# Kernel tuning notes

Hardware: AMD Instinct MI355X
Metric: run time of the kernel (lower is better)

Reference implementation:

```python
import jax, jax.numpy as jnp
import numpy as np

B, S, V, E, H, K = 64, 512, 50000, 128, 256, 20
PAD_IDX, SOS_IDX = 0, 19
NEG = -9999.0


def _lstm_dir(x, mask, W_ih, W_hh, b):
    # x: [B,S,E], mask: [B,S] float. PyTorch gate order: i,f,g,o.
    xg = jnp.einsum('bse,ge->bsg', x, W_ih) + b  # [B,S,4H]

    def step(carry, inp):
        h, c = carry
        xg_t, m = inp  # [B,4H], [B,1]
        g = xg_t + h @ W_hh.T
        i, f, gg, o = jnp.split(g, 4, axis=-1)
        i = jax.nn.sigmoid(i); f = jax.nn.sigmoid(f); o = jax.nn.sigmoid(o)
        gg = jnp.tanh(gg)
        c_new = f * c + i * gg
        h_new = o * jnp.tanh(c_new)
        h = m * h_new + (1.0 - m) * h
        c = m * c_new + (1.0 - m) * c
        return (h, c), h * m  # packed/pad_packed => zeros at padding

    h0 = jnp.zeros((x.shape[0], W_hh.shape[1]), x.dtype)
    _, hs = jax.lax.scan(step, (h0, h0), (xg.transpose(1, 0, 2), mask.T[:, :, None]))
    return hs.transpose(1, 0, 2)  # [B,S,H]


def setup_inputs() -> dict:
    key = jax.random.key(0)
    ks = jax.random.split(key, 12)
    word_seq = jax.random.randint(ks[0], (B, S), 0, V)
    tags = jax.random.randint(ks[1], (B, S), 1, K - 1)  # avoid pad(0) and sos(K-1)
    lengths = S // 2 + jax.random.randint(ks[2], (B,), 0, S // 2)
    sc = 0.1
    embed = jax.random.normal(ks[3], (V, E), jnp.float32) * sc
    W_ih_f = jax.random.normal(ks[4], (4 * H, E), jnp.float32) * sc
    W_hh_f = jax.random.normal(ks[5], (4 * H, H), jnp.float32) * sc
    b_f = jnp.zeros((4 * H,), jnp.float32).at[H:2 * H].set(1.0)  # forget bias 1
    W_ih_b = jax.random.normal(ks[6], (4 * H, E), jnp.float32) * sc
    W_hh_b = jax.random.normal(ks[7], (4 * H, H), jnp.float32) * sc
    b_b = jnp.zeros((4 * H,), jnp.float32).at[H:2 * H].set(1.0)
    lin_W = jax.random.normal(ks[8], (K, 2 * H), jnp.float32) * sc
    lin_b = jnp.zeros((K,), jnp.float32)
    trans = jax.random.normal(ks[9], (K, K), jnp.float32) * 0.1 - 1.0
    trans = trans.at[SOS_IDX, :].set(NEG).at[:, PAD_IDX].set(NEG)
    trans = trans.at[PAD_IDX, :].set(NEG).at[PAD_IDX, PAD_IDX].set(0.0)
    return dict(word_seq=word_seq, tags=tags, lengths=lengths, embed=embed,
                W_ih_f=W_ih_f, W_hh_f=W_hh_f, b_f=b_f,
                W_ih_b=W_ih_b, W_hh_b=W_hh_b, b_b=b_b,
                lin_W=lin_W, lin_b=lin_b, trans=trans)


def reference(word_seq, tags, lengths, embed, W_ih_f, W_hh_f, b_f,
              W_ih_b, W_hh_b, b_b, lin_W, lin_b, trans):
    mask = (jnp.arange(S)[None, :] < lengths[:, None]).astype(jnp.float32)  # [B,S]
    x = embed[word_seq]  # [B,S,E]

    # forward direction
    h_f = _lstm_dir(x, mask, W_ih_f, W_hh_f, b_f)
    # backward direction: reverse within each valid length (packed-seq semantics)
    t = jnp.arange(S)[None, :]
    ri = jnp.where(t < lengths[:, None], lengths[:, None] - 1 - t, t)  # [B,S]
    x_rev = jnp.take_along_axis(x, ri[:, :, None], axis=1)
    h_b_rev = _lstm_dir(x_rev, mask, W_ih_b, W_hh_b, b_b)
    h_b = jnp.take_along_axis(h_b_rev, ri[:, :, None], axis=1)

    rnn_out = jnp.concatenate([h_f, h_b], axis=-1)  # [B,S,2H]
    feats = jnp.einsum('bsd,kd->bsk', rnn_out, lin_W) + lin_b  # [B,S,K]

    # --- CRF numerator: score of gold path ---
    states = jnp.concatenate(
        [jnp.full((B, 1), SOS_IDX, dtype=tags.dtype), tags], axis=1)  # [B,S+1]
    emis = jnp.take_along_axis(feats, tags[:, :, None], axis=-1)[..., 0]  # [B,S]
    trn = trans[states[:, 1:], states[:, :-1]]  # [B,S]
    numerator = jnp.sum((emis + trn) * mask, axis=1)  # [B]

    # --- CRF denominator: forward algorithm (log partition) ---
    score0 = jnp.full((B, K), NEG, jnp.float32).at[:, SOS_IDX].set(0.0)

    def step(score, inp):
        em, m = inp  # [B,K], [B,1]
        new = jax.nn.logsumexp(
            score[:, None, :] + em[:, :, None] + trans[None, :, :], axis=-1)
        score = m * new + (1.0 - m) * score
        return score, None

    score, _ = jax.lax.scan(
        step, score0, (feats.transpose(1, 0, 2), mask.T[:, :, None]))
    denominator = jax.nn.logsumexp(score, axis=-1)  # [B]

    return denominator - numerator  # per-example negative log-likelihood [B]
```

## Files before the change

### kernel.cpp

```cpp
#include <hip/hip_runtime.h>
#include <hip/hip_fp16.h>
#include <stdint.h>

#define BB 64
#define SS 512
#define EE 128
#define HH 256
#define KK 20
#define NEGV -9999.0f
#define SOS_IDX 19

#define VC 18
#define LC 9
#define SC 5

typedef unsigned int u32;

__device__ __forceinline__ float sigm(float x){ return 1.0f / (1.0f + __expf(-x)); }
__device__ __forceinline__ float tanh_fast(float x){
  float e = __expf(2.f * x);
  return 1.f - 2.f / (e + 1.f);
}

__device__ __forceinline__ void pk4(uint4 w, const __half2* hp,
                                    __half2& a0, __half2& a1, __half2& a2, __half2& a3){
  __half2 w0 = *(__half2*)&w.x, w1 = *(__half2*)&w.y, w2 = *(__half2*)&w.z, w3 = *(__half2*)&w.w;
  a0 = __hfma2(w0, hp[0], a0);
  a1 = __hfma2(w1, hp[1], a1);
  a2 = __hfma2(w2, hp[2], a2);
  a3 = __hfma2(w3, hp[3], a3);
}
__device__ __forceinline__ float flushacc(__half2& a0, __half2& a1, __half2& a2, __half2& a3){
  float2 f0 = __half22float2(a0), f1 = __half22float2(a1);
  float2 f2 = __half22float2(a2), f3 = __half22float2(a3);
  __half2 z = __floats2half2_rn(0.f, 0.f);
  a0 = z; a1 = z; a2 = z; a3 = z;
  return ((f0.x + f0.y) + (f1.x + f1.y)) + ((f2.x + f2.y) + (f3.x + f3.y));
}

__global__ void prep_whh(const float* __restrict__ whh_f, const float* __restrict__ whh_b,
                         __half* __restrict__ wp){
  int id = blockIdx.x * 256 + threadIdx.x;
  if (id >= 524288) return;
  int d = id >> 18;
  int rem = id & 262143;
  int row = rem >> 8;
  int k = rem & 255;
  const float* w = d ? whh_b : whh_f;
  wp[(((size_t)d * 32 + (k >> 3)) * 1024 + row) * 8 + (k & 7)] = __float2half(w[row * 256 + k]);
}

__global__ void prep_wih(const float* __restrict__ wih_f, const float* __restrict__ wih_b,
                         float* __restrict__ wt){
  int id = blockIdx.x * 256 + threadIdx.x;
  if (id >= 262144) return;
  int d = id >> 17;
  int rem = id & 131071;
  int col = rem >> 7;
  int k = rem & 127;
  const float* w = d ? wih_b : wih_f;
  wt[(size_t)k * 2048 + d * 1024 + col] = w[col * 128 + k];
}

__global__ __launch_bounds__(256) void xg_gemm(const int* __restrict__ word_seq,
    const int* __restrict__ lengths,
    const float* __restrict__ embed, const float* __restrict__ wt,
    const float* __restrict__ b_f, const float* __restrict__ b_b,
    __half* __restrict__ xg){
  __shared__ __align__(16) float xs[16][128];
  int rb = blockIdx.x >> 1, cb = blockIdx.x & 1;
  {
    int s0 = (rb * 16) & 511, bq = (rb * 16) >> 9;
    if (s0 >= lengths[bq]) return;
  }
  int tid = threadIdx.x;
  {
    int r = tid >> 4, kq = (tid & 15) * 8;
    int bs = rb * 16 + r;
    int w = word_seq[bs];
    const float* er = embed + (size_t)w * 128 + kq;
    float4 a = *(const float4*)er;
    float4 b = *(const float4*)(er + 4);
    *(float4*)&xs[r][kq] = a;
    *(float4*)&xs[r][kq + 4] = b;
  }
  __syncthreads();
  int co = tid * 4;
  const float* bias = cb ? b_b : b_f;
  float4 bv = *(const float4*)(bias + co);
  float4 acc[16];
  #pragma unroll
  for (int r = 0; r < 16; r++) acc[r] = bv;
  const float* wptr = wt + cb * 1024 + co;
  for (int k = 0; k < 128; k++){
    float4 w4 = *(const float4*)(wptr + (size_t)k * 2048);
    #pragma unroll
    for (int r = 0; r < 16; r++){
      float xv = xs[r][k];
      acc[r].x += xv * w4.x; acc[r].y += xv * w4.y;
      acc[r].z += xv * w4.z; acc[r].w += xv * w4.w;
    }
  }
  __half* base = xg + (size_t)cb * ((size_t)BB * SS * 1024);
  #pragma unroll
  for (int r = 0; r < 16; r++){
    int bs = rb * 16 + r;
    __half* o = base + (size_t)bs * 1024 + co;
    __half2 p0 = __floats2half2_rn(acc[r].x, acc[r].y);
    __half2 p1 = __floats2half2_rn(acc[r].z, acc[r].w);
    uint2 st; st.x = *(u32*)&p0; st.y = *(u32*)&p1;
    *(uint2*)o = st;
  }
}

__global__ __launch_bounds__(1024, 4) void lstm_seq(const int* __restrict__ lengths,
    const __half* __restrict__ wp, const __half* __restrict__ xg,
    __half* __restrict__ rnn){
  extern __shared__ __align__(16) char smem[];
  u32*    wl = (u32*)smem;
  float*  gl = (float*)(smem + 147456);
  __half* hb = (__half*)(smem + 151552);

  int bx = blockIdx.x;
  int b = bx & 63, d = bx >> 6;
  int tid = threadIdx.x;
  int u = tid & 255, g = tid >> 8;
  int l = lengths[b];
  const uint4* wp4 = (const uint4*)(wp + (size_t)d * (32 * 1024 * 8));

  uint4 w[VC];
  #pragma unroll
  for (int c = 0; c < VC; c++) w[c] = wp4[c * 1024 + tid];
  #pragma unroll
  for (int c = 0; c < LC; c++)
    *(uint4*)&wl[(c * 1024 + tid) * 4] = wp4[(VC + c) * 1024 + tid];
  if (tid < 256) hb[tid] = __float2half(0.f);
  float cc = 0.f;
  const __half* xgd = xg + ((size_t)d * BB * SS + (size_t)b * SS) * 1024;
  __half* rbp = rnn + (size_t)b * SS * 512 + d * 256;
  int cur = 0;
  __syncthreads();

  for (int t = 0; t < l; t++){
    int s = d ? (l - 1 - t) : t;
    float xv = __half2float(xgd[(size_t)s * 1024 + tid]);
    uint4 sw[SC];
    #pragma unroll
    for (int c = 0; c < SC; c++) sw[c] = wp4[(VC + LC + c) * 1024 + tid];

    const __half* hc = &hb[cur * 256];
    __half2 z = __floats2half2_rn(0.f, 0.f);
    __half2 a0 = z, a1 = z, a2 = z, a3 = z;
    float fa;
    #pragma unroll
    for (int c = 0; c < 16; c++){
      uint4 hv = *(const uint4*)&hc[c * 8];
      pk4(w[c], (const __half2*)&hv, a0, a1, a2, a3);
    }
    fa = flushacc(a0, a1, a2, a3);
    #pragma unroll
    for (int c = 16; c < VC; c++){
      uint4 hv = *(const uint4*)&hc[c * 8];
      pk4(w[c], (const __half2*)&hv, a0, a1, a2, a3);
    }
    #pragma unroll
    for (int c = 0; c < LC; c++){
      uint4 hv = *(const uint4*)&hc[(VC + c) * 8];
      uint4 wv = *(const uint4*)&wl[(c * 1024 + tid) * 4];
      pk4(wv, (const __half2*)&hv, a0, a1, a2, a3);
    }
    #pragma unroll
    for (int c = 0; c < SC; c++){
      uint4 hv = *(const uint4*)&hc[(VC + LC + c) * 8];
      pk4(sw[c], (const __half2*)&hv, a0, a1, a2, a3);
    }
    fa += flushacc(a0, a1, a2, a3);
    fa += xv;

    float gv = (g == 2) ? tanh_fast(fa) : sigm(fa);
    gl[tid] = gv;
    __syncthreads();
    float iv = gl[u], fv = gl[u + 256], ggv = gl[u + 512], ov = gl[u + 768];
    cc = fv * cc + iv * ggv;
    float h = ov * tanh_fast(cc);
    if (g == 0)      hb[(cur ^ 1) * 256 + u] = __float2half(h);
    else if (g == 1) rbp[(size_t)s * 512 + u] = __float2half(h);
    __syncthreads();
    cur ^= 1;
  }
}

__global__ void feat_gemv(const int* __restrict__ lengths,
    const __half* __restrict__ rnn,
    const float* __restrict__ linW, const float* __restrict__ linb,
    float* __restrict__ feats){
  int id = blockIdx.x * 256 + threadIdx.x;
  if (id >= BB * SS * KK) return;
  int row = id / 20;
  int col = id - row * 20;
  int s = row & 511, bq = row >> 9;
  if (s >= lengths[bq]) return;
  const __half* rr = rnn + (size_t)row * 512;
  const float* wr = linW + col * 512;
  float acc = linb[col];
  for (int k8 = 0; k8 < 64; k8++){
    uint4 rv = *(const uint4*)(rr + k8 * 8);
    const __half2* h2 = (const __half2*)&rv;
    float2 p0 = __half22float2(h2[0]);
    float2 p1 = __half22float2(h2[1]);
    float2 p2 = __half22float2(h2[2]);
    float2 p3 = __half22float2(h2[3]);
    float4 wa = *(const float4*)(wr + k8 * 8);
    float4 wb = *(const float4*)(wr + k8 * 8 + 4);
    acc += p0.x * wa.x + p0.y * wa.y + p1.x * wa.z + p1.y * wa.w
         + p2.x * wb.x + p2.y * wb.y + p3.x * wb.z + p3.y * wb.w;
  }
  feats[id] = acc;
}

__global__ __launch_bounds__(64) void crf_kernel(const int* __restrict__ tags,
    const int* __restrict__ lengths, const float* __restrict__ trans,
    const float* __restrict__ feats, float* __restrict__ out){
  int b = blockIdx.x, tid = threadIdx.x;
  __shared__ float tr[400];
  __shared__ float sc[20];
  for (int i = tid; i < 400; i += 64) tr[i] = trans[i];
  __syncthreads();
  int l = lengths[b];
  const int* tg = tags + b * SS;
  const float* fb = feats + (size_t)b * SS * 20;
  float p = 0.f;
  for (int s = tid; s < SS; s += 64){
    if (s < l){
      int cur = tg[s];
      int prev = s ? tg[s - 1] : SOS_IDX;
      p += fb[s * 20 + cur] + tr[cur * 20 + prev];
    }
  }
  #pragma unroll
  for (int off = 32; off; off >>= 1) p += __shfl_down(p, off);
  if (tid < 20) sc[tid] = (tid == SOS_IDX) ? 0.f : NEGV;
  float em = (tid < 20 && l > 0) ? fb[tid] : 0.f;
  for (int s = 0; s < l; s++){
    float em_nxt = (tid < 20 && (s + 1) < l) ? fb[(s + 1) * 20 + tid] : 0.f;
    if (tid < 20){
      const float* trow = &tr[tid * 20];
      float v[20];
      float m = -1e30f;
      #pragma unroll
      for (int jj = 0; jj < 20; jj++){ v[jj] = sc[jj] + trow[jj]; m = fmaxf(m, v[jj]); }
      float ssum = 0.f;
      #pragma unroll
      for (int jj = 0; jj < 20; jj++) ssum += __expf(v[jj] - m);
      sc[tid] = em + m + __logf(ssum);
    }
    em = em_nxt;
  }
  if (tid == 0){
    float m = -1e30f;
    #pragma unroll
    for (int i = 0; i < 20; i++) m = fmaxf(m, sc[i]);
    float ssum = 0.f;
    #pragma unroll
    for (int i = 0; i < 20; i++) ssum += __expf(sc[i] - m);
    out[b] = (m + __logf(ssum)) - p;
  }
}

extern "C" void kernel_launch(void* const* d_in, const int* in_sizes, int n_in,
                              void* d_out, int out_size, void* d_ws, size_t ws_size,
                              hipStream_t stream){
  const int*   word_seq = (const int*)d_in[0];
  const int*   tags     = (const int*)d_in[1];
  const int*   lengths  = (const int*)d_in[2];
  const float* embed    = (const float*)d_in[3];
  const float* wih_f    = (const float*)d_in[4];
  const float* whh_f    = (const float*)d_in[5];
  const float* b_f      = (const float*)d_in[6];
  const float* wih_b    = (const float*)d_in[7];
  const float* whh_b    = (const float*)d_in[8];
  const float* b_b      = (const float*)d_in[9];
  const float* linW     = (const float*)d_in[10];
  const float* linb     = (const float*)d_in[11];
  const float* trans    = (const float*)d_in[12];
  float* out = (float*)d_out;

  char* ws = (char*)d_ws;
  __half* wp    = (__half*)ws;
  float*  wt    = (float*)(ws + (1ull << 20));
  __half* xg    = (__half*)(ws + (2ull << 20));
  __half* rnn   = (__half*)(ws + (2ull << 20) + (128ull << 20));
  float*  feats = (float*)(ws + (2ull << 20) + (160ull << 20));

  (void)hipFuncSetAttribute((const void*)lstm_seq,
        hipFuncAttributeMaxDynamicSharedMemorySize, 152576);

  prep_whh<<<dim3(2048), dim3(256), 0, stream>>>(whh_f, whh_b, wp);
  prep_wih<<<dim3(1024), dim3(256), 0, stream>>>(wih_f, wih_b, wt);
  xg_gemm<<<dim3(4096), dim3(256), 0, stream>>>(word_seq, lengths, embed, wt, b_f, b_b, xg);
  lstm_seq<<<dim3(128), dim3(1024), 152576, stream>>>(lengths, wp, xg, rnn);
  feat_gemv<<<dim3(2560), dim3(256), 0, stream>>>(lengths, rnn, linW, linb, feats);
  crf_kernel<<<dim3(64), dim3(64), 0, stream>>>(tags, lengths, trans, feats, out);
}
```

Measured before the change: 1.690 ms.

## Compute two gate rows per thread in LSTM recurrence, exchange gates via shuffle

The recurrent LSTM kernel moves from 1024 threads (one gate row each) to 512 threads that each compute two gate rows, paired so the i/f/g/o gates for one hidden unit sit in adjacent lanes and are exchanged with __shfl_xor. This drops the shared-memory gate buffer and one __syncthreads per timestep, and tanh is expressed through a scaled sigmoid to avoid divergence. The register/LDS/streamed split of W_hh is rebalanced (more in registers, fewer in LDS) and asm pins keep the weights resident. The cost is higher register pressure per thread and half as many threads to hide latency.

```diff
diff --git a/kernel.cpp b/kernel.cpp
--- a/kernel.cpp
+++ b/kernel.cpp
@@ -10,11 +10,13 @@
 #define NEGV -9999.0f
 #define SOS_IDX 19
 
-#define VC 18
-#define LC 9
+#define VC 20
+#define LC 7
 #define SC 5
 
 typedef unsigned int u32;
+
+#define PIN4(v) asm volatile("" : "+v"((v).x), "+v"((v).y), "+v"((v).z), "+v"((v).w))
 
 __device__ __forceinline__ float sigm(float x){ return 1.0f / (1.0f + __expf(-x)); }
 __device__ __forceinline__ float tanh_fast(float x){
@@ -113,78 +115,100 @@
   }
 }
 
-__global__ __launch_bounds__(1024, 4) void lstm_seq(const int* __restrict__ lengths,
+__global__ __launch_bounds__(512, 2) void lstm_seq(const int* __restrict__ lengths,
     const __half* __restrict__ wp, const __half* __restrict__ xg,
     __half* __restrict__ rnn){
   extern __shared__ __align__(16) char smem[];
   u32*    wl = (u32*)smem;
-  float*  gl = (float*)(smem + 147456);
-  __half* hb = (__half*)(smem + 151552);
+  __half* hb = (__half*)(smem + 114688);
 
   int bx = blockIdx.x;
   int b = bx & 63, d = bx >> 6;
   int tid = threadIdx.x;
-  int u = tid & 255, g = tid >> 8;
+  int u = tid >> 1, q = tid & 1;
+  int row0 = u + q * 256;
+  int row1 = row0 + 512;
   int l = lengths[b];
   const uint4* wp4 = (const uint4*)(wp + (size_t)d * (32 * 1024 * 8));
 
-  uint4 w[VC];
-  #pragma unroll
-  for (int c = 0; c < VC; c++) w[c] = wp4[c * 1024 + tid];
-  #pragma unroll
-  for (int c = 0; c < LC; c++)
-    *(uint4*)&wl[(c * 1024 + tid) * 4] = wp4[(VC + c) * 1024 + tid];
+  uint4 w0[VC], w1[VC];
+  #pragma unroll
+  for (int c = 0; c < VC; c++){ w0[c] = wp4[c * 1024 + row0]; w1[c] = wp4[c * 1024 + row1]; }
+  #pragma unroll
+  for (int c = 0; c < VC; c++){ PIN4(w0[c]); PIN4(w1[c]); }
+  #pragma unroll
+  for (int c = 0; c < LC; c++){
+    *(uint4*)&wl[((c * 2 + 0) * 512 + tid) * 4] = wp4[(VC + c) * 1024 + row0];
+    *(uint4*)&wl[((c * 2 + 1) * 512 + tid) * 4] = wp4[(VC + c) * 1024 + row1];
+  }
   if (tid < 256) hb[tid] = __float2half(0.f);
   float cc = 0.f;
   const __half* xgd = xg + ((size_t)d * BB * SS + (size_t)b * SS) * 1024;
   __half* rbp = rnn + (size_t)b * SS * 512 + d * 256;
+  float nsc = q ? 1.f : 2.f;
+  float nmu = q ? 1.f : 2.f;
+  float nad = q ? 0.f : -1.f;
   int cur = 0;
   __syncthreads();
 
   for (int t = 0; t < l; t++){
     int s = d ? (l - 1 - t) : t;
-    float xv = __half2float(xgd[(size_t)s * 1024 + tid]);
-    uint4 sw[SC];
-    #pragma unroll
-    for (int c = 0; c < SC; c++) sw[c] = wp4[(VC + LC + c) * 1024 + tid];
-
+    const __half* xr = xgd + (size_t)s * 1024;
+    float xv0 = __half2float(xr[row0]);
+    float xv1 = __half2float(xr[row1]);
+    uint4 s0[SC], s1[SC];
+    #pragma unroll
+    for (int c = 0; c < SC; c++){
+      s0[c] = wp4[(VC + LC + c) * 1024 + row0];
+      s1[c] = wp4[(VC + LC + c) * 1024 + row1];
+    }
     const __half* hc = &hb[cur * 256];
     __half2 z = __floats2half2_rn(0.f, 0.f);
-    __half2 a0 = z, a1 = z, a2 = z, a3 = z;
-    float fa;
-    #pragma unroll
-    for (int c = 0; c < 16; c++){
+    __half2 a00 = z, a01 = z, a02 = z, a03 = z;
+    __half2 a10 = z, a11 = z, a12 = z, a13 = z;
+    float fa0, fa1;
+    #pragma unroll
+    for (int c = 0; c < VC; c++){
       uint4 hv = *(const uint4*)&hc[c * 8];
-      pk4(w[c], (const __half2*)&hv, a0, a1, a2, a3);
-    }
-    fa = flushacc(a0, a1, a2, a3);
-    #pragma unroll
-    for (int c = 16; c < VC; c++){
-      uint4 hv = *(const uint4*)&hc[c * 8];
-      pk4(w[c], (const __half2*)&hv, a0, a1, a2, a3);
-    }
+      const __half2* hp = (const __half2*)&hv;
+      pk4(w0[c], hp, a00, a01, a02, a03);
+      pk4(w1[c], hp, a10, a11, a12, a13);
+    }
+    fa0 = flushacc(a00, a01, a02, a03);
+    fa1 = flushacc(a10, a11, a12, a13);
     #pragma unroll
     for (int c = 0; c < LC; c++){
       uint4 hv = *(const uint4*)&hc[(VC + c) * 8];
-      uint4 wv = *(const uint4*)&wl[(c * 1024 + tid) * 4];
-      pk4(wv, (const __half2*)&hv, a0, a1, a2, a3);
+      const __half2* hp = (const __half2*)&hv;
+      uint4 v0 = *(const uint4*)&wl[((c * 2 + 0) * 512 + tid) * 4];
+      uint4 v1 = *(const uint4*)&wl[((c * 2 + 1) * 512 + tid) * 4];
+      pk4(v0, hp, a00, a01, a02, a03);
+      pk4(v1, hp, a10, a11, a12, a13);
     }
     #pragma unroll
     for (int c = 0; c < SC; c++){
       uint4 hv = *(const uint4*)&hc[(VC + LC + c) * 8];
-      pk4(sw[c], (const __half2*)&hv, a0, a1, a2, a3);
-    }
-    fa += flushacc(a0, a1, a2, a3);
-    fa += xv;
-
-    float gv = (g == 2) ? tanh_fast(fa) : sigm(fa);
-    gl[tid] = gv;
-    __syncthreads();
-    float iv = gl[u], fv = gl[u + 256], ggv = gl[u + 512], ov = gl[u + 768];
-    cc = fv * cc + iv * ggv;
+      const __half2* hp = (const __half2*)&hv;
+      pk4(s0[c], hp, a00, a01, a02, a03);
+      pk4(s1[c], hp, a10, a11, a12, a13);
+    }
+    fa0 += flushacc(a00, a01, a02, a03);
+    fa1 += flushacc(a10, a11, a12, a13);
+
+    fa0 += xv0;
+    fa1 += xv1;
+    float g0 = sigm(fa0);
+    float g1 = sigm(nsc * fa1) * nmu + nad;
+    float p0 = __shfl_xor(g0, 1);
+    float p1 = __shfl_xor(g1, 1);
+    float iv = q ? p0 : g0;
+    float fv = q ? g0 : p0;
+    float gv = q ? p1 : g1;
+    float ov = q ? g1 : p1;
+    cc = fv * cc + iv * gv;
     float h = ov * tanh_fast(cc);
-    if (g == 0)      hb[(cur ^ 1) * 256 + u] = __float2half(h);
-    else if (g == 1) rbp[(size_t)s * 512 + u] = __float2half(h);
+    if (q) rbp[(size_t)s * 512 + u] = __float2half(h);
+    else   hb[(cur ^ 1) * 256 + u] = __float2half(h);
     __syncthreads();
     cur ^= 1;
   }
@@ -293,12 +317,12 @@
   float*  feats = (float*)(ws + (2ull << 20) + (160ull << 20));
 
   (void)hipFuncSetAttribute((const void*)lstm_seq,
-        hipFuncAttributeMaxDynamicSharedMemorySize, 152576);
+        hipFuncAttributeMaxDynamicSharedMemorySize, 115712);
 
   prep_whh<<<dim3(2048), dim3(256), 0, stream>>>(whh_f, whh_b, wp);
   prep_wih<<<dim3(1024), dim3(256), 0, stream>>>(wih_f, wih_b, wt);
   xg_gemm<<<dim3(4096), dim3(256), 0, stream>>>(word_seq, lengths, embed, wt, b_f, b_b, xg);
-  lstm_seq<<<dim3(128), dim3(1024), 152576, stream>>>(lengths, wp, xg, rnn);
+  lstm_seq<<<dim3(128), dim3(512), 115712, stream>>>(lengths, wp, xg, rnn);
   feat_gemv<<<dim3(2560), dim3(256), 0, stream>>>(lengths, rnn, linW, linb, feats);
   crf_kernel<<<dim3(64), dim3(64), 0, stream>>>(tags, lengths, trans, feats, out);
 }
```

Result: no change. 1.663 ms (-1.6%).
